# Kernel tuning notes

Measured on AMD Instinct MI355X. Metric: run time of the kernel, lower is better.

The kernel has to match this reference:

```python
import jax, jax.numpy as jnp
import numpy as np

H = 8          # n_heads
M = 16         # max_dist
U = 512        # n_units
DH = U // H    # d_head
EPS = 1e-3     # keras LayerNormalization default epsilon
NEG = -2.0**32 + 1.0


def _rel_table(pe, T):
    # pe: [2M+1, DH]; returns [T, T, DH] with rel[i, j] = pe[clip(j - i, -M, M) + M]
    i = jnp.arange(T)
    idx = jnp.clip(i[None, :] - i[:, None], -M, M) + M
    return pe[idx]


def _split_heads(x):
    # [B, T, U] -> [H*B, T, DH]  (head-major, matching tf.concat(tf.split(x, H, 2), 0))
    B, T, _ = x.shape
    return x.reshape(B, T, H, DH).transpose(2, 0, 1, 3).reshape(H * B, T, DH)


def _merge_heads(x, B):
    # [H*B, T, DH] -> [B, T, U]
    T = x.shape[1]
    return x.reshape(H, B, T, DH).transpose(1, 2, 0, 3).reshape(B, T, U)


def setup_inputs() -> dict:
    key = jax.random.key(0)
    ks = jax.random.split(key, 10)
    B, T = 8, 1024
    s = 1.0 / np.sqrt(U)
    inp = {
        'q': jax.random.normal(ks[0], (B, T, U), jnp.float32),
        'k': jax.random.normal(ks[1], (B, T, U), jnp.float32),
        'v': jax.random.normal(ks[2], (B, T, U), jnp.float32),
        'Wq': jax.random.normal(ks[3], (U, U), jnp.float32) * s,
        'bq': jnp.zeros((U,), jnp.float32),
        'Wk': jax.random.normal(ks[4], (U, U), jnp.float32) * s,
        'bk': jnp.zeros((U,), jnp.float32),
        'Wv': jax.random.normal(ks[5], (U, U), jnp.float32) * s,
        'bv': jnp.zeros((U,), jnp.float32),
        'Wo': jax.random.normal(ks[6], (U, U), jnp.float32) * s,
        'bo': jnp.zeros((U,), jnp.float32),
        'gamma': jnp.ones((U,), jnp.float32),
        'beta': jnp.zeros((U,), jnp.float32),
        'pe_k': jax.random.normal(ks[7], (2 * M + 1, DH), jnp.float32) * 0.05,
        'pe_v': jax.random.normal(ks[8], (2 * M + 1, DH), jnp.float32) * 0.05,
    }
    return inp


def reference(q, k, v, Wq, bq, Wk, bk, Wv, bv, Wo, bo, gamma, beta, pe_k, pe_v):
    B, T, _ = q.shape
    relu = jax.nn.relu
    q_emb = relu(q @ Wq + bq)
    k_emb = relu(k @ Wk + bk)
    v_emb = relu(v @ Wv + bv)
    qh = _split_heads(q_emb)   # [HB, T, DH]
    kh = _split_heads(k_emb)
    vh = _split_heads(v_emb)

    attn = jnp.einsum('btd,bsd->bts', qh, kh)
    rel_k = _rel_table(pe_k, T)                       # [T, T, DH]
    attn = attn + jnp.einsum('btd,tsd->bts', qh, rel_k)
    attn = attn / jnp.asarray(DH, attn.dtype) ** 0.5

    causal = jnp.tril(jnp.ones((T, T), jnp.bool_))
    attn = jnp.where(causal[None], attn, jnp.asarray(NEG, attn.dtype))
    w = jax.nn.softmax(attn, axis=-1)

    out = jnp.einsum('bts,bsd->btd', w, vh)
    rel_v = _rel_table(pe_v, T)
    out = out + jnp.einsum('bts,tsd->btd', w, rel_v)

    out = _merge_heads(out, B)                        # [B, T, U]
    out = relu(out @ Wo + bo)
    out = out + q

    mu = jnp.mean(out, axis=-1, keepdims=True)
    var = jnp.mean(jnp.square(out - mu), axis=-1, keepdims=True)
    return (out - mu) * jax.lax.rsqrt(var + EPS) * gamma + beta
```

## Files before the change

kernel.cpp:

```cpp
#include <hip/hip_runtime.h>
#include <hip/hip_bf16.h>

#define T_SEQ 1024
#define U_DIM 512
#define LN_EPS 1e-3f
#define LOG2E 1.44269504f

typedef float  f32x4  __attribute__((ext_vector_type(4)));
typedef short  bf16x8 __attribute__((ext_vector_type(8)));

__device__ __forceinline__ unsigned short f2bf(float f) {
    union { float f; unsigned u; } x; x.f = f;
    unsigned r = x.u + 0x7fffu + ((x.u >> 16) & 1u);
    return (unsigned short)(r >> 16);
}
__device__ __forceinline__ float b2f(short s) {
    union { unsigned u; float f; } x; x.u = ((unsigned)(unsigned short)s) << 16;
    return x.f;
}
__device__ __forceinline__ int packbf(float a, float b) {
    return (int)((unsigned)f2bf(a) | ((unsigned)f2bf(b) << 16));
}
__device__ __forceinline__ void async_copy16(void* lds, const void* g) {
    __builtin_amdgcn_global_load_lds((const __attribute__((address_space(1))) void*)g,
                                     (__attribute__((address_space(3))) void*)lds, 16, 0, 0);
}

#define WAITV(N) asm volatile("s_waitcnt vmcnt(" #N ")" ::: "memory")

__global__ __launch_bounds__(256) void prep_all(
        const float* __restrict__ Wq, const float* __restrict__ Wk,
        const float* __restrict__ Wv, const float* __restrict__ Wo,
        short* __restrict__ wt,
        const float* __restrict__ q, const float* __restrict__ k, const float* __restrict__ v,
        short* __restrict__ qb, short* __restrict__ kb, short* __restrict__ vb) {
    __shared__ float Ws[64][65];
    const int bid = blockIdx.x, t = threadIdx.x;
    if (bid >= 256) {
        const size_t off = ((size_t)(bid - 256) * 256 + t) * 8;
#pragma unroll
        for (int z = 0; z < 3; ++z) {
            const float* src = (z == 0) ? q : (z == 1) ? k : v;
            short* dst = (z == 0) ? qb : (z == 1) ? kb : vb;
            float4 a = *(const float4*)(src + off);
            float4 b = *(const float4*)(src + off + 4);
            int4 o;
            o.x = packbf(a.x, a.y);
            o.y = packbf(a.z, a.w);
            o.z = packbf(b.x, b.y);
            o.w = packbf(b.z, b.w);
            *(int4*)(dst + off) = o;
        }
        return;
    }
    const int z = bid >> 6, tile = bid & 63;
    const float* W = (z == 0) ? Wq : (z == 1) ? Wk : (z == 2) ? Wv : Wo;
    short* Wt = wt + (size_t)z * 262144;
    const int k0 = (tile >> 3) * 64, n0 = (tile & 7) * 64;
    {
        const int kr = t >> 2, cs = (t & 3) * 16;
        const float4* src = (const float4*)(W + (size_t)(k0 + kr) * 512 + n0 + cs);
#pragma unroll
        for (int i = 0; i < 4; ++i) {
            float4 vv = src[i];
            Ws[kr][cs + 4 * i + 0] = vv.x;
            Ws[kr][cs + 4 * i + 1] = vv.y;
            Ws[kr][cs + 4 * i + 2] = vv.z;
            Ws[kr][cs + 4 * i + 3] = vv.w;
        }
    }
    __syncthreads();
    {
        const int nr = t >> 2, ks = (t & 3) * 16;
        int4 w0, w1;
        w0.x = packbf(Ws[ks + 0][nr], Ws[ks + 1][nr]);
        w0.y = packbf(Ws[ks + 2][nr], Ws[ks + 3][nr]);
        w0.z = packbf(Ws[ks + 4][nr], Ws[ks + 5][nr]);
        w0.w = packbf(Ws[ks + 6][nr], Ws[ks + 7][nr]);
        w1.x = packbf(Ws[ks + 8][nr], Ws[ks + 9][nr]);
        w1.y = packbf(Ws[ks + 10][nr], Ws[ks + 11][nr]);
        w1.z = packbf(Ws[ks + 12][nr], Ws[ks + 13][nr]);
        w1.w = packbf(Ws[ks + 14][nr], Ws[ks + 15][nr]);
        short* dst = Wt + (size_t)(n0 + nr) * 512 + k0 + ks;
        *(int4*)dst = w0;
        *(int4*)(dst + 8) = w1;
    }
}

template <int OUT, int BM, int BN>
__global__ __launch_bounds__(256) void gemm_mfma(
        const void* __restrict__ A0, const void* __restrict__ A1, const void* __restrict__ A2,
        const short* __restrict__ Wt0, const short* __restrict__ Wt1, const short* __restrict__ Wt2,
        const float* __restrict__ b0p, const float* __restrict__ b1p, const float* __restrict__ b2p,
        const float* __restrict__ resid,
        void* __restrict__ O0, void* __restrict__ O1, void* __restrict__ O2) {
    constexpr int ASZ = BM * 32;
    constexpr int BSZ = BN * 32;
    constexpr int TSZ = ASZ + BSZ;
    constexpr int NA  = BM / 16;
    constexpr int NB  = BN / 16;
    constexpr int MW  = BM / 64;
    constexpr int NW  = 4 / MW;
    constexpr int AJ  = BN / (16 * NW);
    constexpr int LPW = (NA + NB) / 4;
    static_assert((NA + NB) % 4 == 0, "cells divisible by waves");
    __shared__ short Ls[4 * TSZ];

    const int z = blockIdx.z;
    const void* Av = (z == 0) ? A0 : (z == 1) ? A1 : A2;
    const short* Wz = (z == 0) ? Wt0 : (z == 1) ? Wt1 : Wt2;
    const float* bz = (z == 0) ? b0p : (z == 1) ? b1p : b2p;
    void* Ov = (z == 0) ? O0 : (z == 1) ? O1 : O2;

    const int tid = threadIdx.x;
    const int m0 = blockIdx.x * BM, n0 = blockIdx.y * BN;
    const int w = tid >> 6, lane = tid & 63;
    const int n15 = lane & 15, g = lane >> 4;
    const int mh = w / NW, nh = w % NW;

    f32x4 acc[4][AJ];
#pragma unroll
    for (int i = 0; i < 4; ++i)
#pragma unroll
        for (int j = 0; j < AJ; ++j) acc[i][j] = (f32x4){0.f, 0.f, 0.f, 0.f};

    const short* gsrc[LPW];
    int loff[LPW];
#pragma unroll
    for (int cl = 0; cl < LPW; ++cl) {
        const int cid = w * LPW + cl;
        if (cid < NA) {
            gsrc[cl] = (const short*)Av + (size_t)(m0 + cid * 16 + n15) * 512 + g * 8;
            loff[cl] = cid * 512;
        } else {
            const int c2 = cid - NA;
            gsrc[cl] = Wz + (size_t)(n0 + c2 * 16 + n15) * 512 + g * 8;
            loff[cl] = ASZ + c2 * 512;
        }
    }

#define STAGE(CK, BUF)                                                                   \
    do {                                                                                 \
        _Pragma("unroll")                                                                \
        for (int cl = 0; cl < LPW; ++cl)                                                 \
            async_copy16(Ls + (BUF) * TSZ + loff[cl], gsrc[cl] + (CK) * 32);             \
    } while (0)

    STAGE(0, 0);
    STAGE(1, 1);
    STAGE(2, 2);

    for (int ck = 0; ck < 16; ++ck) {
        if (ck < 14) {
            if constexpr (LPW == 3) WAITV(6); else WAITV(4);
        } else if (ck == 14) {
            if constexpr (LPW == 3) WAITV(3); else WAITV(2);
        } else {
            WAITV(0);
        }
        __builtin_amdgcn_s_barrier();
        __builtin_amdgcn_sched_barrier(0);
        if (ck + 3 <= 15) STAGE(ck + 3, (ck + 3) & 3);
        const int cb = ck & 3;
        bf16x8 af[4], bfv[AJ];
#pragma unroll
        for (int i = 0; i < 4; ++i)
            af[i] = *(const bf16x8*)(Ls + cb * TSZ + (mh * 4 + i) * 512 + lane * 8);
#pragma unroll
        for (int j = 0; j < AJ; ++j)
            bfv[j] = *(const bf16x8*)(Ls + cb * TSZ + ASZ + (nh * AJ + j) * 512 + lane * 8);
#pragma unroll
        for (int i = 0; i < 4; ++i)
#pragma unroll
            for (int j = 0; j < AJ; ++j)
                acc[i][j] = __builtin_amdgcn_mfma_f32_16x16x32_bf16(af[i], bfv[j], acc[i][j], 0, 0, 0);
    }
#undef STAGE

    const int mbase = m0 + mh * 64 + g * 4;
    const int nbase = n0 + nh * (AJ * 16) + n15;
    const bool even = (n15 & 1) == 0;
    float bj[AJ];
#pragma unroll
    for (int j = 0; j < AJ; ++j) bj[j] = bz[nbase + j * 16];

#pragma unroll
    for (int i = 0; i < 4; ++i) {
        const int mrow = mbase + i * 16;
#pragma unroll
        for (int j = 0; j < AJ; ++j) {
            const int ncol = nbase + j * 16;
            f32x4 a = acc[i][j];
            float v0 = fmaxf(a[0] + bj[j], 0.f);
            float v1 = fmaxf(a[1] + bj[j], 0.f);
            float v2 = fmaxf(a[2] + bj[j], 0.f);
            float v3 = fmaxf(a[3] + bj[j], 0.f);
            if (OUT == 0) {
                unsigned t01 = (unsigned)packbf(v0, v1);
                unsigned t23 = (unsigned)packbf(v2, v3);
                unsigned x01 = (unsigned)__shfl_xor((int)t01, 1, 64);
                unsigned x23 = (unsigned)__shfl_xor((int)t23, 1, 64);
                short* Oz = (short*)Ov;
                if (even) {
                    unsigned d0 = (t01 & 0xffffu) | (x01 << 16);
                    unsigned d1 = (t01 >> 16) | (x01 & 0xffff0000u);
                    *(unsigned*)(Oz + (size_t)(mrow + 0) * 512 + ncol) = d0;
                    *(unsigned*)(Oz + (size_t)(mrow + 1) * 512 + ncol) = d1;
                } else {
                    unsigned d2 = (x23 & 0xffffu) | (t23 << 16);
                    unsigned d3 = (x23 >> 16) | (t23 & 0xffff0000u);
                    *(unsigned*)(Oz + (size_t)(mrow + 2) * 512 + ncol - 1) = d2;
                    *(unsigned*)(Oz + (size_t)(mrow + 3) * 512 + ncol - 1) = d3;
                }
            } else {
                float x0 = __shfl_xor(v0, 1, 64);
                float x1 = __shfl_xor(v1, 1, 64);
                float x2 = __shfl_xor(v2, 1, 64);
                float x3 = __shfl_xor(v3, 1, 64);
                float* Oz = (float*)Ov;
                if (even) {
                    float2 r0 = *(const float2*)(resid + (size_t)(mrow + 0) * 512 + ncol);
                    float2 r1 = *(const float2*)(resid + (size_t)(mrow + 1) * 512 + ncol);
                    *(float2*)(Oz + (size_t)(mrow + 0) * 512 + ncol) = make_float2(v0 + r0.x, x0 + r0.y);
                    *(float2*)(Oz + (size_t)(mrow + 1) * 512 + ncol) = make_float2(v1 + r1.x, x1 + r1.y);
                } else {
                    float2 r2 = *(const float2*)(resid + (size_t)(mrow + 2) * 512 + ncol - 1);
                    float2 r3 = *(const float2*)(resid + (size_t)(mrow + 3) * 512 + ncol - 1);
                    *(float2*)(Oz + (size_t)(mrow + 2) * 512 + ncol - 1) = make_float2(x2 + r2.x, v2 + r2.y);
                    *(float2*)(Oz + (size_t)(mrow + 3) * 512 + ncol - 1) = make_float2(x3 + r3.x, v3 + r3.y);
                }
            }
        }
    }
}

__global__ __launch_bounds__(256) void attn_mfma(
        const short* __restrict__ qe, const short* __restrict__ ke,
        const short* __restrict__ ve, const float* __restrict__ pe_k,
        float* __restrict__ ml, short* __restrict__ ao) {
    __shared__ short Kc[2 * 4096];
    __shared__ short Vc[2 * 4096];
    __shared__ float qpeS[4 * 16 * 17];

    const int tid = threadIdx.x;
    const int bid = blockIdx.x;
    const int q4 = bid >> 8, r4 = bid & 3;
    const int rank = (q4 < 2) ? (r4 + 4 * q4) : (15 - (r4 + 4 * (q4 - 2)));
    const int hb = (bid >> 2) & 63;
    const int tt = 15 - rank;
    const int h = hb >> 3, b = hb & 7;
    const int w = tid >> 6, lane = tid & 63;
    const int g = lane >> 4, n15 = lane & 15;
    const int sp = tid & 31, dbase = (tid >> 5) * 8;
    float* qpeW = qpeS + w * (16 * 17);

    const size_t rowbase = (size_t)b * T_SEQ;

    int qn = 0;
    bf16x8 Bq[2];
    float qpe0 = 0.f;
    float m_r = -1.0e38f, l_r = 0.f, m2 = -1.4427e38f;
    f32x4 oacc[4];

#define SETUP(TILE)                                                                      \
    do {                                                                                 \
        qn = (TILE) * 64 + w * 16;                                                       \
        _Pragma("unroll")                                                                \
        for (int kh = 0; kh < 2; ++kh) {                                                 \
            bf16x8 t = *(const bf16x8*)(qe + (rowbase + qn + n15) * U_DIM + h * 64 + kh * 32 + g * 8); \
            _Pragma("unroll")                                                            \
            for (int i2 = 0; i2 < 8; ++i2) {                                             \
                unsigned short u = (unsigned short)t[i2];                                \
                t[i2] = (short)(((u & 0x7f80u) > 0x0180u) ? (unsigned short)(u - 0x0180u) \
                                                          : (unsigned short)(u & 0x8000u)); \
            }                                                                            \
            Bq[kh] = t;                                                                  \
        }                                                                                \
        f32x4 qa[2];                                                                     \
        qa[0] = (f32x4){0.f, 0.f, 0.f, 0.f};                                             \
        qa[1] = (f32x4){0.f, 0.f, 0.f, 0.f};                                             \
        _Pragma("unroll")                                                                \
        for (int mt = 0; mt < 2; ++mt)                                                   \
        _Pragma("unroll")                                                                \
        for (int kh = 0; kh < 2; ++kh) {                                                 \
            const float* src = pe_k + (mt * 16 + n15) * 64 + kh * 32 + g * 8;            \
            float4 f0 = *(const float4*)src;                                             \
            float4 f1 = *(const float4*)(src + 4);                                       \
            bf16x8 fr;                                                                   \
            fr[0] = (short)f2bf(f0.x); fr[1] = (short)f2bf(f0.y);                        \
            fr[2] = (short)f2bf(f0.z); fr[3] = (short)f2bf(f0.w);                        \
            fr[4] = (short)f2bf(f1.x); fr[5] = (short)f2bf(f1.y);                        \
            fr[6] = (short)f2bf(f1.z); fr[7] = (short)f2bf(f1.w);                        \
            qa[mt] = __builtin_amdgcn_mfma_f32_16x16x32_bf16(fr, Bq[kh], qa[mt], 0, 0, 0); \
        }                                                                                \
        _Pragma("unroll")                                                                \
        for (int mt = 0; mt < 2; ++mt)                                                   \
        _Pragma("unroll")                                                                \
        for (int r = 0; r < 4; ++r) {                                                    \
            const int ri = mt * 16 + 4 * g + r;                                          \
            if (ri <= 16) qpeW[n15 * 17 + ri] = qa[mt][r];                               \
        }                                                                                \
        qpe0 = qpeW[n15 * 17];                                                           \
        m_r = -1.0e38f; l_r = 0.f; m2 = -1.4427e38f;                                     \
        _Pragma("unroll")                                                                \
        for (int dt = 0; dt < 4; ++dt) oacc[dt] = (f32x4){0.f, 0.f, 0.f, 0.f};           \
    } while (0)

#define STAGE_K(S, BUF)                                                                  \
    do {                                                                                 \
        _Pragma("unroll")                                                                \
        for (int j = 0; j < 2; ++j) {                                                    \
            const int cc = w * 2 + j, kh = cc >> 2, mt = cc & 3;                         \
            const short* gp = ke + (rowbase + (S) + mt * 16 + n15) * U_DIM + h * 64 + kh * 32 + g * 8; \
            async_copy16(Kc + (BUF) * 4096 + cc * 512, gp);                              \
        }                                                                                \
    } while (0)

#define LOAD_V(S)                                                                        \
    do {                                                                                 \
        const short* r0 = ve + (rowbase + (S) + 2 * sp) * U_DIM + h * 64 + dbase;        \
        vx = *(const bf16x8*)r0;                                                         \
        vy = *(const bf16x8*)(r0 + U_DIM);                                               \
    } while (0)

#define STORE_V(BUF)                                                                     \
    do {                                                                                 \
        const int vkh = sp >> 4, vg = (sp & 15) >> 2, vj = (sp & 3) * 2;                 \
        _Pragma("unroll")                                                                \
        for (int i = 0; i < 8; ++i) {                                                    \
            const int d = dbase + i;                                                     \
            int pv = (int)((unsigned short)vx[i]) | (((int)(unsigned short)vy[i]) << 16);\
            *(int*)(Vc + (BUF) * 4096 + (vkh * 4 + (d >> 4)) * 512 + ((d & 15) + 16 * vg) * 8 + vj) = pv; \
        }                                                                                \
    } while (0)

    SETUP(tt);
    bf16x8 vx, vy;
    STAGE_K(0, 0);
    LOAD_V(0);
    STORE_V(0);

    for (int gs = 0; gs <= tt; ++gs) {
        const int cb = gs & 1, nb = cb ^ 1;
        const int s0 = gs * 64;
        __syncthreads();
        if (gs < tt) {
            STAGE_K((gs + 1) * 64, nb);
            LOAD_V((gs + 1) * 64);
        }

        {
            int cls[4];
#pragma unroll
            for (int mt = 0; mt < 4; ++mt) {
                const int slo = s0 + mt * 16;
                cls[mt] = (slo > qn + 15) ? 0 : ((slo + 31 < qn) ? 1 : 2);
            }
            f32x4 c[4];
#pragma unroll
            for (int mt = 0; mt < 4; ++mt) c[mt] = (f32x4){0.f, 0.f, 0.f, 0.f};
            __builtin_amdgcn_s_setprio(1);
#pragma unroll
            for (int mt = 0; mt < 4; ++mt) {
                if (!cls[mt]) continue;
#pragma unroll
                for (int kh = 0; kh < 2; ++kh) {
                    bf16x8 ak = *(const bf16x8*)(Kc + cb * 4096 + (kh * 4 + mt) * 512 + lane * 8);
                    c[mt] = __builtin_amdgcn_mfma_f32_16x16x32_bf16(ak, Bq[kh], c[mt], 0, 0, 0);
                }
            }
            __builtin_amdgcn_s_setprio(0);

            const int qg = qn + n15;
            float sc[4][4];
            float pmax = -3.0e38f;
#pragma unroll
            for (int mt = 0; mt < 4; ++mt) {
                if (cls[mt] == 0) {
#pragma unroll
                    for (int r = 0; r < 4; ++r) sc[mt][r] = -3.0e38f;
                } else if (cls[mt] == 1) {
#pragma unroll
                    for (int r = 0; r < 4; ++r) {
                        sc[mt][r] = c[mt][r] + qpe0;
                        pmax = fmaxf(pmax, sc[mt][r]);
                    }
                } else {
#pragma unroll
                    for (int r = 0; r < 4; ++r) {
                        const int sg = s0 + mt * 16 + 4 * g + r;
                        const int dlt = sg - qg;
                        if (dlt <= 0) {
                            const int ri = (dlt < -16) ? 0 : (dlt + 16);
                            sc[mt][r] = c[mt][r] + qpeW[n15 * 17 + ri];
                            pmax = fmaxf(pmax, sc[mt][r]);
                        } else {
                            sc[mt][r] = -3.0e38f;
                        }
                    }
                }
            }
            pmax = fmaxf(pmax, __shfl_xor(pmax, 16, 64));
            pmax = fmaxf(pmax, __shfl_xor(pmax, 32, 64));

            const bool resc = __any(pmax > m_r + 8.0f);
            float alpha = 1.0f;
            if (resc) {
                const float mnew = fmaxf(m_r, pmax);
                alpha = __expf(m_r - mnew);
                m_r = mnew;
                m2 = mnew * LOG2E;
            }
            float p[4][4];
            float psum = 0.f;
#pragma unroll
            for (int mt = 0; mt < 4; ++mt)
#pragma unroll
            for (int r = 0; r < 4; ++r) {
                const float pv = (cls[mt] == 0) ? 0.f
                                : exp2f(fmaf(sc[mt][r], LOG2E, -m2));
                p[mt][r] = pv;
                psum += pv;
            }
            psum += __shfl_xor(psum, 16, 64);
            psum += __shfl_xor(psum, 32, 64);
            l_r = l_r * alpha + psum;

            int pk01[4], pk23[4];
#pragma unroll
            for (int mt = 0; mt < 4; ++mt) {
                asm("v_cvt_pk_bf16_f32 %0, %1, %2" : "=v"(pk01[mt]) : "v"(p[mt][0]), "v"(p[mt][1]));
                asm("v_cvt_pk_bf16_f32 %0, %1, %2" : "=v"(pk23[mt]) : "v"(p[mt][2]), "v"(p[mt][3]));
            }
            const int srcA = ((g & 1) * 2) * 16 + n15;
            const int srcB = srcA + 16;
            const bool selHi = (g >> 1) != 0;
            if (resc) {
                float aO[4];
#pragma unroll
                for (int r = 0; r < 4; ++r) aO[r] = __shfl(alpha, 4 * g + r, 64);
#pragma unroll
                for (int dt = 0; dt < 4; ++dt)
#pragma unroll
                for (int r = 0; r < 4; ++r) oacc[dt][r] *= aO[r];
            }
#pragma unroll
            for (int kh = 0; kh < 2; ++kh) {
                if (cls[2 * kh] == 0 && cls[2 * kh + 1] == 0) continue;
                const int a0l = __shfl(pk01[2 * kh], srcA, 64);
                const int a0h = __shfl(pk01[2 * kh + 1], srcA, 64);
                const int a1l = __shfl(pk23[2 * kh], srcA, 64);
                const int a1h = __shfl(pk23[2 * kh + 1], srcA, 64);
                const int a2l = __shfl(pk01[2 * kh], srcB, 64);
                const int a2h = __shfl(pk01[2 * kh + 1], srcB, 64);
                const int a3l = __shfl(pk23[2 * kh], srcB, 64);
                const int a3h = __shfl(pk23[2 * kh + 1], srcB, 64);
                union { int i[4]; bf16x8 v; } au;
                au.i[0] = selHi ? a0h : a0l;
                au.i[1] = selHi ? a1h : a1l;
                au.i[2] = selHi ? a2h : a2l;
                au.i[3] = selHi ? a3h : a3l;
                __builtin_amdgcn_s_setprio(1);
#pragma unroll
                for (int dt = 0; dt < 4; ++dt) {
                    bf16x8 bv = *(const bf16x8*)(Vc + cb * 4096 + (kh * 4 + dt) * 512 + lane * 8);
                    oacc[dt] = __builtin_amdgcn_mfma_f32_16x16x32_bf16(au.v, bv, oacc[dt], 0, 0, 0);
                }
                __builtin_amdgcn_s_setprio(0);
            }
        }

        if (gs < tt) STORE_V(nb);
    }

    if (g == 0)
        *(float2*)(ml + ((size_t)hb * T_SEQ + qn + n15) * 2) = make_float2(m_r, l_r);
#pragma unroll
    for (int r = 0; r < 4; ++r) {
        const float lq = __shfl(l_r, 4 * g + r, 64);
        const float linv = 1.0f / lq;
        short* dst = ao + (rowbase + qn + 4 * g + r) * U_DIM + h * 64 + n15;
#pragma unroll
        for (int dt = 0; dt < 4; ++dt)
            dst[dt * 16] = (short)f2bf(oacc[dt][r] * linv);
    }
#undef SETUP
#undef STAGE_K
#undef LOAD_V
#undef STORE_V
}

__global__ __launch_bounds__(256) void band_relv(
        const short* __restrict__ qe, const short* __restrict__ ke,
        const float* __restrict__ pe_k, const float* __restrict__ pe_v,
        const float* __restrict__ ml, short* __restrict__ ao) {
    __shared__ float pek[17 * 64];
    __shared__ float pev[17 * 64];
    const int tb = blockIdx.x, hb = blockIdx.y;
    const int h = hb >> 3, b = hb & 7;
    const int tid = threadIdx.x;
    for (int i = tid; i < 17 * 64; i += 256) {
        pek[i] = b2f((short)f2bf(pe_k[i]));
        pev[i] = pe_v[i];
    }
    __syncthreads();

    const int t = tb * 64 + (tid >> 2);
    const int p = (tid & 3) * 16;
    const short* qp = qe + (size_t)(b * T_SEQ + t) * U_DIM + h * 64 + p;
    bf16x8 qa = *(const bf16x8*)qp, qb2 = *(const bf16x8*)(qp + 8);
    float qv[16];
#pragma unroll
    for (int i = 0; i < 8; ++i) { qv[i] = b2f(qa[i]); qv[8 + i] = b2f(qb2[i]); }

    float dots[17];
#pragma unroll
    for (int ri = 0; ri < 17; ++ri) {
        const int s = t - 16 + ri;
        float acc = 0.f;
        if (s >= 0) {
            const short* kp = ke + (size_t)(b * T_SEQ + s) * U_DIM + h * 64 + p;
            bf16x8 ka = *(const bf16x8*)kp, kb2 = *(const bf16x8*)(kp + 8);
#pragma unroll
            for (int d = 0; d < 8; ++d) {
                acc += qv[d] * b2f(ka[d]);
                acc += qv[8 + d] * b2f(kb2[d]);
            }
#pragma unroll
            for (int d = 0; d < 16; ++d) acc += qv[d] * pek[ri * 64 + p + d];
        }
        dots[ri] = acc;
    }
#pragma unroll
    for (int ri = 0; ri < 17; ++ri) {
        dots[ri] += __shfl_xor(dots[ri], 1, 64);
        dots[ri] += __shfl_xor(dots[ri], 2, 64);
    }

    const float2 mlv = *(const float2*)(ml + ((size_t)hb * T_SEQ + t) * 2);
    const float m = mlv.x, linv = 1.0f / mlv.y;
    float wv[17];
    float wsum = 0.f;
#pragma unroll
    for (int ri = 0; ri < 17; ++ri) {
        const int s = t - 16 + ri;
        const float wr = (s >= 0) ? __expf(dots[ri] * 0.125f - m) * linv : 0.f;
        wv[ri] = wr;
        wsum += wr;
    }
    wv[0] += 1.0f - wsum;

    float relv[16];
#pragma unroll
    for (int d = 0; d < 16; ++d) relv[d] = 0.f;
#pragma unroll
    for (int ri = 0; ri < 17; ++ri)
#pragma unroll
        for (int d = 0; d < 16; ++d) relv[d] += wv[ri] * pev[ri * 64 + p + d];

    short* op = ao + (size_t)(b * T_SEQ + t) * U_DIM + h * 64 + p;
    bf16x8 a0 = *(const bf16x8*)op, a1 = *(const bf16x8*)(op + 8);
    int4 o0, o1;
    o0.x = packbf(b2f(a0[0]) + relv[0],  b2f(a0[1]) + relv[1]);
    o0.y = packbf(b2f(a0[2]) + relv[2],  b2f(a0[3]) + relv[3]);
    o0.z = packbf(b2f(a0[4]) + relv[4],  b2f(a0[5]) + relv[5]);
    o0.w = packbf(b2f(a0[6]) + relv[6],  b2f(a0[7]) + relv[7]);
    o1.x = packbf(b2f(a1[0]) + relv[8],  b2f(a1[1]) + relv[9]);
    o1.y = packbf(b2f(a1[2]) + relv[10], b2f(a1[3]) + relv[11]);
    o1.z = packbf(b2f(a1[4]) + relv[12], b2f(a1[5]) + relv[13]);
    o1.w = packbf(b2f(a1[6]) + relv[14], b2f(a1[7]) + relv[15]);
    *(int4*)op = o0;
    *(int4*)(op + 8) = o1;
}

__global__ __launch_bounds__(256) void ln_kernel(float* __restrict__ io,
                                                 const float* __restrict__ gamma,
                                                 const float* __restrict__ beta) {
    const int row = blockIdx.x * 4 + (threadIdx.x >> 6);
    const int lane = threadIdx.x & 63;
    float* rp = io + (size_t)row * 512 + lane * 8;
    float4 a = *(const float4*)rp;
    float4 c = *(const float4*)(rp + 4);
    float v[8] = {a.x, a.y, a.z, a.w, c.x, c.y, c.z, c.w};

    float s = v[0] + v[1] + v[2] + v[3] + v[4] + v[5] + v[6] + v[7];
#pragma unroll
    for (int off = 1; off < 64; off <<= 1) s += __shfl_xor(s, off, 64);
    const float mu = s * (1.0f / 512.0f);

    float sq = 0.f;
#pragma unroll
    for (int i = 0; i < 8; ++i) { v[i] -= mu; sq += v[i] * v[i]; }
#pragma unroll
    for (int off = 1; off < 64; off <<= 1) sq += __shfl_xor(sq, off, 64);
    const float rs = rsqrtf(sq * (1.0f / 512.0f) + LN_EPS);

    const float4 g0 = *(const float4*)(gamma + lane * 8);
    const float4 g1 = *(const float4*)(gamma + lane * 8 + 4);
    const float4 b0 = *(const float4*)(beta + lane * 8);
    const float4 b1 = *(const float4*)(beta + lane * 8 + 4);
    float4 o0, o1;
    o0.x = v[0] * rs * g0.x + b0.x;
    o0.y = v[1] * rs * g0.y + b0.y;
    o0.z = v[2] * rs * g0.z + b0.z;
    o0.w = v[3] * rs * g0.w + b0.w;
    o1.x = v[4] * rs * g1.x + b1.x;
    o1.y = v[5] * rs * g1.y + b1.y;
    o1.z = v[6] * rs * g1.z + b1.z;
    o1.w = v[7] * rs * g1.w + b1.w;
    *(float4*)rp = o0;
    *(float4*)(rp + 4) = o1;
}

extern "C" void kernel_launch(void* const* d_in, const int* in_sizes, int n_in,
                              void* d_out, int out_size, void* d_ws, size_t ws_size,
                              hipStream_t stream) {
    const float* q     = (const float*)d_in[0];
    const float* k     = (const float*)d_in[1];
    const float* v     = (const float*)d_in[2];
    const float* Wq    = (const float*)d_in[3];
    const float* bq    = (const float*)d_in[4];
    const float* Wk    = (const float*)d_in[5];
    const float* bk    = (const float*)d_in[6];
    const float* Wv    = (const float*)d_in[7];
    const float* bv    = (const float*)d_in[8];
    const float* Wo    = (const float*)d_in[9];
    const float* bo    = (const float*)d_in[10];
    const float* gamma = (const float*)d_in[11];
    const float* beta  = (const float*)d_in[12];
    const float* pe_k  = (const float*)d_in[13];
    const float* pe_v  = (const float*)d_in[14];
    float* out = (float*)d_out;

    char* base = (char*)d_ws;
    short* qe = (short*)(base);
    short* ke = (short*)(base + (((size_t)8) << 20));
    short* ve = (short*)(base + (((size_t)16) << 20));
    short* ao = (short*)(base + (((size_t)24) << 20));
    short* wt = (short*)(base + (((size_t)32) << 20));
    float* ml = (float*)(base + (((size_t)34) << 20));
    short* qb = (short*)(base + (((size_t)36) << 20));
    short* kb = (short*)(base + (((size_t)44) << 20));
    short* vb = (short*)(base + (((size_t)52) << 20));
    short* wtq = wt, *wtk = wt + 262144, *wtv = wt + 2 * 262144, *wto = wt + 3 * 262144;

    prep_all<<<dim3(2304), 256, 0, stream>>>(Wq, Wk, Wv, Wo, wt, q, k, v, qb, kb, vb);
    gemm_mfma<0, 128, 64><<<dim3(64, 8, 3), 256, 0, stream>>>(
        qb, kb, vb, wtq, wtk, wtv, bq, bk, bv, nullptr, qe, ke, ve);
    attn_mfma<<<dim3(1024), 256, 0, stream>>>(qe, ke, ve, pe_k, ml, ao);
    band_relv<<<dim3(16, 64), 256, 0, stream>>>(qe, ke, pe_k, pe_v, ml, ao);
    gemm_mfma<1, 64, 64><<<dim3(128, 8, 1), 256, 0, stream>>>(
        ao, ao, ao, wto, wto, wto, bo, bo, bo, q, out, out, out);
    ln_kernel<<<dim3(2048), 256, 0, stream>>>(out, gamma, beta);
}
```

Measured before the change: 252.6 us.

## Split attention KV range across two blocks per query tile and combine

Each query tile's causal key range is split into two halves handled by separate blocks (flash-decoding style split-K), doubling the grid to 2048 blocks for better load balance across CUs. A new combine kernel merges the partial outputs using the per-row max and sum statistics, writing the merged ml for band_relv. The output GEMM tile shape also changes to 64x128 with half the grid. This adds an extra kernel launch plus global traffic for the partial results, and reuses the qb/kb buffers as scratch.

```diff
diff --git a/kernel.cpp b/kernel.cpp
--- a/kernel.cpp
+++ b/kernel.cpp
@@ -237,17 +237,23 @@
 __global__ __launch_bounds__(256) void attn_mfma(
         const short* __restrict__ qe, const short* __restrict__ ke,
         const short* __restrict__ ve, const float* __restrict__ pe_k,
-        float* __restrict__ ml, short* __restrict__ ao) {
+        float* __restrict__ ml1, float* __restrict__ ml2,
+        short* __restrict__ ao, short* __restrict__ ao2) {
     __shared__ short Kc[2 * 4096];
     __shared__ short Vc[2 * 4096];
     __shared__ float qpeS[4 * 16 * 17];
 
     const int tid = threadIdx.x;
     const int bid = blockIdx.x;
-    const int q4 = bid >> 8, r4 = bid & 3;
-    const int rank = (q4 < 2) ? (r4 + 4 * q4) : (15 - (r4 + 4 * (q4 - 2)));
-    const int hb = (bid >> 2) & 63;
-    const int tt = 15 - rank;
+    const int cu = bid & 255, chunk = bid >> 8;
+    const int hb = cu >> 2, r4 = cu & 3;
+    int tt, half;
+    if (chunk < 4) { tt = 4 * r4 + chunk;              half = 0; }
+    else           { tt = 15 - 4 * r4 - (chunk - 4);   half = 1; }
+    const int n0h = (tt + 2) >> 1;
+    const int g0 = half ? n0h : 0;
+    const int g1 = half ? (tt + 1) : n0h;
+
     const int h = hb >> 3, b = hb & 7;
     const int w = tid >> 6, lane = tid & 63;
     const int g = lane >> 4, n15 = lane & 15;
@@ -255,56 +261,62 @@
     float* qpeW = qpeS + w * (16 * 17);
 
     const size_t rowbase = (size_t)b * T_SEQ;
-
-    int qn = 0;
+    short* aoP = half ? ao2 : ao;
+    float* mlP = half ? ml2 : ml1;
+
+    int qn = tt * 64 + w * 16;
+
+    if (g0 >= g1) {
+        if (g == 0)
+            *(float2*)(mlP + ((size_t)hb * T_SEQ + qn + n15) * 2) = make_float2(-3.0e38f, 0.f);
+        return;
+    }
+
     bf16x8 Bq[2];
     float qpe0 = 0.f;
     float m_r = -1.0e38f, l_r = 0.f, m2 = -1.4427e38f;
     f32x4 oacc[4];
 
-#define SETUP(TILE)                                                                      \
-    do {                                                                                 \
-        qn = (TILE) * 64 + w * 16;                                                       \
-        _Pragma("unroll")                                                                \
-        for (int kh = 0; kh < 2; ++kh) {                                                 \
-            bf16x8 t = *(const bf16x8*)(qe + (rowbase + qn + n15) * U_DIM + h * 64 + kh * 32 + g * 8); \
-            _Pragma("unroll")                                                            \
-            for (int i2 = 0; i2 < 8; ++i2) {                                             \
-                unsigned short u = (unsigned short)t[i2];                                \
-                t[i2] = (short)(((u & 0x7f80u) > 0x0180u) ? (unsigned short)(u - 0x0180u) \
-                                                          : (unsigned short)(u & 0x8000u)); \
-            }                                                                            \
-            Bq[kh] = t;                                                                  \
-        }                                                                                \
-        f32x4 qa[2];                                                                     \
-        qa[0] = (f32x4){0.f, 0.f, 0.f, 0.f};                                             \
-        qa[1] = (f32x4){0.f, 0.f, 0.f, 0.f};                                             \
-        _Pragma("unroll")                                                                \
-        for (int mt = 0; mt < 2; ++mt)                                                   \
-        _Pragma("unroll")                                                                \
-        for (int kh = 0; kh < 2; ++kh) {                                                 \
-            const float* src = pe_k + (mt * 16 + n15) * 64 + kh * 32 + g * 8;            \
-            float4 f0 = *(const float4*)src;                                             \
-            float4 f1 = *(const float4*)(src + 4);                                       \
-            bf16x8 fr;                                                                   \
-            fr[0] = (short)f2bf(f0.x); fr[1] = (short)f2bf(f0.y);                        \
-            fr[2] = (short)f2bf(f0.z); fr[3] = (short)f2bf(f0.w);                        \
-            fr[4] = (short)f2bf(f1.x); fr[5] = (short)f2bf(f1.y);                        \
-            fr[6] = (short)f2bf(f1.z); fr[7] = (short)f2bf(f1.w);                        \
-            qa[mt] = __builtin_amdgcn_mfma_f32_16x16x32_bf16(fr, Bq[kh], qa[mt], 0, 0, 0); \
-        }                                                                                \
-        _Pragma("unroll")                                                                \
-        for (int mt = 0; mt < 2; ++mt)                                                   \
-        _Pragma("unroll")                                                                \
-        for (int r = 0; r < 4; ++r) {                                                    \
-            const int ri = mt * 16 + 4 * g + r;                                          \
-            if (ri <= 16) qpeW[n15 * 17 + ri] = qa[mt][r];                               \
-        }                                                                                \
-        qpe0 = qpeW[n15 * 17];                                                           \
-        m_r = -1.0e38f; l_r = 0.f; m2 = -1.4427e38f;                                     \
-        _Pragma("unroll")                                                                \
-        for (int dt = 0; dt < 4; ++dt) oacc[dt] = (f32x4){0.f, 0.f, 0.f, 0.f};           \
-    } while (0)
+    {
+#pragma unroll
+        for (int kh = 0; kh < 2; ++kh) {
+            bf16x8 t = *(const bf16x8*)(qe + (rowbase + qn + n15) * U_DIM + h * 64 + kh * 32 + g * 8);
+#pragma unroll
+            for (int i2 = 0; i2 < 8; ++i2) {
+                unsigned short u = (unsigned short)t[i2];
+                t[i2] = (short)(((u & 0x7f80u) > 0x0180u) ? (unsigned short)(u - 0x0180u)
+                                                          : (unsigned short)(u & 0x8000u));
+            }
+            Bq[kh] = t;
+        }
+        f32x4 qa[2];
+        qa[0] = (f32x4){0.f, 0.f, 0.f, 0.f};
+        qa[1] = (f32x4){0.f, 0.f, 0.f, 0.f};
+#pragma unroll
+        for (int mt = 0; mt < 2; ++mt)
+#pragma unroll
+        for (int kh = 0; kh < 2; ++kh) {
+            const float* src = pe_k + (mt * 16 + n15) * 64 + kh * 32 + g * 8;
+            float4 f0 = *(const float4*)src;
+            float4 f1 = *(const float4*)(src + 4);
+            bf16x8 fr;
+            fr[0] = (short)f2bf(f0.x); fr[1] = (short)f2bf(f0.y);
+            fr[2] = (short)f2bf(f0.z); fr[3] = (short)f2bf(f0.w);
+            fr[4] = (short)f2bf(f1.x); fr[5] = (short)f2bf(f1.y);
+            fr[6] = (short)f2bf(f1.z); fr[7] = (short)f2bf(f1.w);
+            qa[mt] = __builtin_amdgcn_mfma_f32_16x16x32_bf16(fr, Bq[kh], qa[mt], 0, 0, 0);
+        }
+#pragma unroll
+        for (int mt = 0; mt < 2; ++mt)
+#pragma unroll
+        for (int r = 0; r < 4; ++r) {
+            const int ri = mt * 16 + 4 * g + r;
+            if (ri <= 16) qpeW[n15 * 17 + ri] = qa[mt][r];
+        }
+        qpe0 = qpeW[n15 * 17];
+#pragma unroll
+        for (int dt = 0; dt < 4; ++dt) oacc[dt] = (f32x4){0.f, 0.f, 0.f, 0.f};
+    }
 
 #define STAGE_K(S, BUF)                                                                  \
     do {                                                                                 \
@@ -334,17 +346,16 @@
         }                                                                                \
     } while (0)
 
-    SETUP(tt);
     bf16x8 vx, vy;
-    STAGE_K(0, 0);
-    LOAD_V(0);
-    STORE_V(0);
-
-    for (int gs = 0; gs <= tt; ++gs) {
+    STAGE_K(g0 * 64, g0 & 1);
+    LOAD_V(g0 * 64);
+    STORE_V(g0 & 1);
+
+    for (int gs = g0; gs < g1; ++gs) {
         const int cb = gs & 1, nb = cb ^ 1;
         const int s0 = gs * 64;
         __syncthreads();
-        if (gs < tt) {
+        if (gs + 1 < g1) {
             STAGE_K((gs + 1) * 64, nb);
             LOAD_V((gs + 1) * 64);
         }
@@ -470,24 +481,63 @@
             }
         }
 
-        if (gs < tt) STORE_V(nb);
+        if (gs + 1 < g1) STORE_V(nb);
     }
 
     if (g == 0)
-        *(float2*)(ml + ((size_t)hb * T_SEQ + qn + n15) * 2) = make_float2(m_r, l_r);
+        *(float2*)(mlP + ((size_t)hb * T_SEQ + qn + n15) * 2) = make_float2(m_r, l_r);
 #pragma unroll
     for (int r = 0; r < 4; ++r) {
         const float lq = __shfl(l_r, 4 * g + r, 64);
-        const float linv = 1.0f / lq;
-        short* dst = ao + (rowbase + qn + 4 * g + r) * U_DIM + h * 64 + n15;
+        const float linv = (lq > 0.f) ? 1.0f / lq : 0.f;
+        short* dst = aoP + (rowbase + qn + 4 * g + r) * U_DIM + h * 64 + n15;
 #pragma unroll
         for (int dt = 0; dt < 4; ++dt)
             dst[dt * 16] = (short)f2bf(oacc[dt][r] * linv);
     }
-#undef SETUP
 #undef STAGE_K
 #undef LOAD_V
 #undef STORE_V
+}
+
+__global__ __launch_bounds__(256) void attn_combine(
+        const float* __restrict__ ml1, const float* __restrict__ ml2,
+        const short* __restrict__ ao2, short* __restrict__ ao,
+        float* __restrict__ ml) {
+    const int R = blockIdx.x * 64 + (threadIdx.x >> 2);
+    const int hb = R >> 10, t = R & 1023;
+    const int h = hb >> 3, b = hb & 7;
+    const int d0 = (threadIdx.x & 3) * 16;
+    const float2 p1 = *(const float2*)(ml1 + (size_t)R * 2);
+    const float2 p2 = *(const float2*)(ml2 + (size_t)R * 2);
+    const float m = fmaxf(p1.x, p2.x);
+    const float w1 = p1.y * __expf(p1.x - m);
+    const float w2 = (p2.y > 0.f) ? p2.y * __expf(p2.x - m) : 0.f;
+    const float inv = 1.0f / (w1 + w2);
+    const float a1 = w1 * inv, a2 = w2 * inv;
+    const size_t off = (size_t)(b * T_SEQ + t) * U_DIM + h * 64 + d0;
+    short* op = ao + off;
+    const short* o2p = ao2 + off;
+    bf16x8 x0 = *(const bf16x8*)op, x1 = *(const bf16x8*)(op + 8);
+    bf16x8 y0 = *(const bf16x8*)o2p, y1 = *(const bf16x8*)(o2p + 8);
+    const bool has2 = (w2 > 0.f);
+    float o[16];
+#pragma unroll
+    for (int i = 0; i < 8; ++i) {
+        float t0 = a1 * b2f(x0[i]);
+        float t1 = a1 * b2f(x1[i]);
+        o[i]     = has2 ? (t0 + a2 * b2f(y0[i])) : t0;
+        o[8 + i] = has2 ? (t1 + a2 * b2f(y1[i])) : t1;
+    }
+    int4 o0, o1;
+    o0.x = packbf(o[0], o[1]);   o0.y = packbf(o[2], o[3]);
+    o0.z = packbf(o[4], o[5]);   o0.w = packbf(o[6], o[7]);
+    o1.x = packbf(o[8], o[9]);   o1.y = packbf(o[10], o[11]);
+    o1.z = packbf(o[12], o[13]); o1.w = packbf(o[14], o[15]);
+    *(int4*)op = o0;
+    *(int4*)(op + 8) = o1;
+    if ((threadIdx.x & 3) == 0)
+        *(float2*)(ml + (size_t)R * 2) = make_float2(m, w1 + w2);
 }
 
 __global__ __launch_bounds__(256) void band_relv(
@@ -639,17 +689,21 @@
     short* ao = (short*)(base + (((size_t)24) << 20));
     short* wt = (short*)(base + (((size_t)32) << 20));
     float* ml = (float*)(base + (((size_t)34) << 20));
+    float* ml1 = (float*)(base + (((size_t)35) << 20));
     short* qb = (short*)(base + (((size_t)36) << 20));
     short* kb = (short*)(base + (((size_t)44) << 20));
     short* vb = (short*)(base + (((size_t)52) << 20));
+    short* ao2 = qb;
+    float* ml2 = (float*)kb;
     short* wtq = wt, *wtk = wt + 262144, *wtv = wt + 2 * 262144, *wto = wt + 3 * 262144;
 
     prep_all<<<dim3(2304), 256, 0, stream>>>(Wq, Wk, Wv, Wo, wt, q, k, v, qb, kb, vb);
     gemm_mfma<0, 128, 64><<<dim3(64, 8, 3), 256, 0, stream>>>(
         qb, kb, vb, wtq, wtk, wtv, bq, bk, bv, nullptr, qe, ke, ve);
-    attn_mfma<<<dim3(1024), 256, 0, stream>>>(qe, ke, ve, pe_k, ml, ao);
+    attn_mfma<<<dim3(2048), 256, 0, stream>>>(qe, ke, ve, pe_k, ml1, ml2, ao, ao2);
+    attn_combine<<<dim3(1024), 256, 0, stream>>>(ml1, ml2, ao2, ao, ml);
     band_relv<<<dim3(16, 64), 256, 0, stream>>>(qe, ke, pe_k, pe_v, ml, ao);
-    gemm_mfma<1, 64, 64><<<dim3(128, 8, 1), 256, 0, stream>>>(
+    gemm_mfma<1, 64, 128><<<dim3(128, 4, 1), 256, 0, stream>>>(
         ao, ao, ao, wto, wto, wto, bo, bo, bo, q, out, out, out);
     ln_kernel<<<dim3(2048), 256, 0, stream>>>(out, gamma, beta);
 }
```

After: 262.0 us. 1.04x slower.

## Fuse fp32-to-bf16 input conversion into QKV projection GEMM

Applied to the files above, without the earlier changes.

Removes the separate pass that converted q/k/v to bf16 and instead loads fp32 activations directly in a new GEMM kernel. That kernel converts them to bf16 in registers while staging into LDS, double-buffered against async weight loads, with 128x128 tiles. The output projection becomes a dedicated non-template-branch kernel with a 64x128 tile, and the attention setup macro is inlined. This saves one full write and read of the bf16 activation copies, but the A path now uses register-staged loads instead of async copies.

```diff
diff --git a/kernel.cpp b/kernel.cpp
--- a/kernel.cpp
+++ b/kernel.cpp
@@ -28,31 +28,12 @@
 
 #define WAITV(N) asm volatile("s_waitcnt vmcnt(" #N ")" ::: "memory")
 
-__global__ __launch_bounds__(256) void prep_all(
+__global__ __launch_bounds__(256) void prep_wt(
         const float* __restrict__ Wq, const float* __restrict__ Wk,
         const float* __restrict__ Wv, const float* __restrict__ Wo,
-        short* __restrict__ wt,
-        const float* __restrict__ q, const float* __restrict__ k, const float* __restrict__ v,
-        short* __restrict__ qb, short* __restrict__ kb, short* __restrict__ vb) {
+        short* __restrict__ wt) {
     __shared__ float Ws[64][65];
     const int bid = blockIdx.x, t = threadIdx.x;
-    if (bid >= 256) {
-        const size_t off = ((size_t)(bid - 256) * 256 + t) * 8;
-#pragma unroll
-        for (int z = 0; z < 3; ++z) {
-            const float* src = (z == 0) ? q : (z == 1) ? k : v;
-            short* dst = (z == 0) ? qb : (z == 1) ? kb : vb;
-            float4 a = *(const float4*)(src + off);
-            float4 b = *(const float4*)(src + off + 4);
-            int4 o;
-            o.x = packbf(a.x, a.y);
-            o.y = packbf(a.z, a.w);
-            o.z = packbf(b.x, b.y);
-            o.w = packbf(b.z, b.w);
-            *(int4*)(dst + off) = o;
-        }
-        return;
-    }
     const int z = bid >> 6, tile = bid & 63;
     const float* W = (z == 0) ? Wq : (z == 1) ? Wk : (z == 2) ? Wv : Wo;
     short* Wt = wt + (size_t)z * 262144;
@@ -87,13 +68,142 @@
     }
 }
 
-template <int OUT, int BM, int BN>
-__global__ __launch_bounds__(256) void gemm_mfma(
-        const void* __restrict__ A0, const void* __restrict__ A1, const void* __restrict__ A2,
+__global__ __launch_bounds__(256) void gemm_cvt(
+        const float* __restrict__ A0, const float* __restrict__ A1, const float* __restrict__ A2,
         const short* __restrict__ Wt0, const short* __restrict__ Wt1, const short* __restrict__ Wt2,
         const float* __restrict__ b0p, const float* __restrict__ b1p, const float* __restrict__ b2p,
-        const float* __restrict__ resid,
-        void* __restrict__ O0, void* __restrict__ O1, void* __restrict__ O2) {
+        short* __restrict__ O0, short* __restrict__ O1, short* __restrict__ O2) {
+    __shared__ short As[2 * 8192];
+    __shared__ short Bs[2 * 8192];
+
+    const int z = blockIdx.z;
+    const float* Av = (z == 0) ? A0 : (z == 1) ? A1 : A2;
+    const short* Wz = (z == 0) ? Wt0 : (z == 1) ? Wt1 : Wt2;
+    const float* bz = (z == 0) ? b0p : (z == 1) ? b1p : b2p;
+    short* Ov = (z == 0) ? O0 : (z == 1) ? O1 : O2;
+
+    const int tid = threadIdx.x;
+    const int m0 = blockIdx.x * 128, n0 = blockIdx.y * 128;
+    const int w = tid >> 6, lane = tid & 63;
+    const int n15 = lane & 15, g = lane >> 4;
+    const int mh = w >> 1, nh = w & 1;
+    const int lr = tid >> 4, c4 = tid & 15;
+
+    f32x4 acc[4][4];
+#pragma unroll
+    for (int i = 0; i < 4; ++i)
+#pragma unroll
+        for (int j = 0; j < 4; ++j) acc[i][j] = (f32x4){0.f, 0.f, 0.f, 0.f};
+
+    float4 areg[8];
+
+#define LOAD_A(CK)                                                                       \
+    do {                                                                                 \
+        const float* abase = Av + (size_t)(m0 + lr) * 512 + (CK) * 64 + c4 * 4;          \
+        _Pragma("unroll")                                                                \
+        for (int i = 0; i < 8; ++i) areg[i] = *(const float4*)(abase + (size_t)8192 * i); \
+    } while (0)
+
+#define STORE_A(BUF)                                                                     \
+    do {                                                                                 \
+        short* sb = As + (BUF) * 8192 + (c4 >> 3) * 8 * 512 + lr * 8 +                   \
+                    ((c4 & 7) >> 1) * 128 + (c4 & 1) * 4;                                \
+        _Pragma("unroll")                                                                \
+        for (int i = 0; i < 8; ++i) {                                                    \
+            int2 wv;                                                                     \
+            wv.x = packbf(areg[i].x, areg[i].y);                                         \
+            wv.y = packbf(areg[i].z, areg[i].w);                                         \
+            *(int2*)(sb + i * 512) = wv;                                                 \
+        }                                                                                \
+    } while (0)
+
+#define STAGE_B(CK, BUF)                                                                 \
+    do {                                                                                 \
+        if (w < 2) {                                                                     \
+            _Pragma("unroll")                                                            \
+            for (int i = 0; i < 8; ++i) {                                                \
+                const int kc = i >> 2, nt = w * 4 + (i & 3);                             \
+                const short* gp = Wz + (size_t)(n0 + nt * 16 + n15) * 512 + (CK) * 64 + kc * 32 + g * 8; \
+                async_copy16(Bs + (BUF) * 8192 + (kc * 8 + nt) * 512, gp);               \
+            }                                                                            \
+        }                                                                                \
+    } while (0)
+
+    LOAD_A(0);
+    STORE_A(0);
+    STAGE_B(0, 0);
+    LOAD_A(1);
+
+    for (int ck = 0; ck < 8; ++ck) {
+        const int cb = ck & 1, nb = cb ^ 1;
+        __syncthreads();
+        if (ck < 7) STAGE_B(ck + 1, nb);
+#pragma unroll
+        for (int kc = 0; kc < 2; ++kc) {
+            bf16x8 af[4], bfv[4];
+#pragma unroll
+            for (int i = 0; i < 4; ++i)
+                af[i] = *(const bf16x8*)(As + cb * 8192 + (kc * 8 + mh * 4 + i) * 512 + lane * 8);
+#pragma unroll
+            for (int j = 0; j < 4; ++j)
+                bfv[j] = *(const bf16x8*)(Bs + cb * 8192 + (kc * 8 + nh * 4 + j) * 512 + lane * 8);
+#pragma unroll
+            for (int i = 0; i < 4; ++i)
+#pragma unroll
+                for (int j = 0; j < 4; ++j)
+                    acc[i][j] = __builtin_amdgcn_mfma_f32_16x16x32_bf16(af[i], bfv[j], acc[i][j], 0, 0, 0);
+        }
+        if (ck < 7) {
+            STORE_A(nb);
+            if (ck < 6) LOAD_A(ck + 2);
+        }
+    }
+#undef LOAD_A
+#undef STORE_A
+#undef STAGE_B
+
+    const int mbase = m0 + mh * 64 + g * 4;
+    const int nbase = n0 + nh * 64 + n15;
+    const bool even = (n15 & 1) == 0;
+    float bj[4];
+#pragma unroll
+    for (int j = 0; j < 4; ++j) bj[j] = bz[nbase + j * 16];
+
+#pragma unroll
+    for (int i = 0; i < 4; ++i) {
+        const int mrow = mbase + i * 16;
+#pragma unroll
+        for (int j = 0; j < 4; ++j) {
+            const int ncol = nbase + j * 16;
+            f32x4 a = acc[i][j];
+            float v0 = fmaxf(a[0] + bj[j], 0.f);
+            float v1 = fmaxf(a[1] + bj[j], 0.f);
+            float v2 = fmaxf(a[2] + bj[j], 0.f);
+            float v3 = fmaxf(a[3] + bj[j], 0.f);
+            unsigned t01 = (unsigned)packbf(v0, v1);
+            unsigned t23 = (unsigned)packbf(v2, v3);
+            unsigned x01 = (unsigned)__shfl_xor((int)t01, 1, 64);
+            unsigned x23 = (unsigned)__shfl_xor((int)t23, 1, 64);
+            if (even) {
+                unsigned d0 = (t01 & 0xffffu) | (x01 << 16);
+                unsigned d1 = (t01 >> 16) | (x01 & 0xffff0000u);
+                *(unsigned*)(Ov + (size_t)(mrow + 0) * 512 + ncol) = d0;
+                *(unsigned*)(Ov + (size_t)(mrow + 1) * 512 + ncol) = d1;
+            } else {
+                unsigned d2 = (x23 & 0xffffu) | (t23 << 16);
+                unsigned d3 = (x23 >> 16) | (t23 & 0xffff0000u);
+                *(unsigned*)(Ov + (size_t)(mrow + 2) * 512 + ncol - 1) = d2;
+                *(unsigned*)(Ov + (size_t)(mrow + 3) * 512 + ncol - 1) = d3;
+            }
+        }
+    }
+}
+
+template <int BM, int BN>
+__global__ __launch_bounds__(256) void gemm_pipe(
+        const short* __restrict__ Ab, const short* __restrict__ Wz,
+        const float* __restrict__ bz, const float* __restrict__ resid,
+        float* __restrict__ Oz) {
     constexpr int ASZ = BM * 32;
     constexpr int BSZ = BN * 32;
     constexpr int TSZ = ASZ + BSZ;
@@ -106,12 +216,6 @@
     static_assert((NA + NB) % 4 == 0, "cells divisible by waves");
     __shared__ short Ls[4 * TSZ];
 
-    const int z = blockIdx.z;
-    const void* Av = (z == 0) ? A0 : (z == 1) ? A1 : A2;
-    const short* Wz = (z == 0) ? Wt0 : (z == 1) ? Wt1 : Wt2;
-    const float* bz = (z == 0) ? b0p : (z == 1) ? b1p : b2p;
-    void* Ov = (z == 0) ? O0 : (z == 1) ? O1 : O2;
-
     const int tid = threadIdx.x;
     const int m0 = blockIdx.x * BM, n0 = blockIdx.y * BN;
     const int w = tid >> 6, lane = tid & 63;
@@ -130,7 +234,7 @@
     for (int cl = 0; cl < LPW; ++cl) {
         const int cid = w * LPW + cl;
         if (cid < NA) {
-            gsrc[cl] = (const short*)Av + (size_t)(m0 + cid * 16 + n15) * 512 + g * 8;
+            gsrc[cl] = Ab + (size_t)(m0 + cid * 16 + n15) * 512 + g * 8;
             loff[cl] = cid * 512;
         } else {
             const int c2 = cid - NA;
@@ -195,40 +299,20 @@
             float v1 = fmaxf(a[1] + bj[j], 0.f);
             float v2 = fmaxf(a[2] + bj[j], 0.f);
             float v3 = fmaxf(a[3] + bj[j], 0.f);
-            if (OUT == 0) {
-                unsigned t01 = (unsigned)packbf(v0, v1);
-                unsigned t23 = (unsigned)packbf(v2, v3);
-                unsigned x01 = (unsigned)__shfl_xor((int)t01, 1, 64);
-                unsigned x23 = (unsigned)__shfl_xor((int)t23, 1, 64);
-                short* Oz = (short*)Ov;
-                if (even) {
-                    unsigned d0 = (t01 & 0xffffu) | (x01 << 16);
-                    unsigned d1 = (t01 >> 16) | (x01 & 0xffff0000u);
-                    *(unsigned*)(Oz + (size_t)(mrow + 0) * 512 + ncol) = d0;
-                    *(unsigned*)(Oz + (size_t)(mrow + 1) * 512 + ncol) = d1;
-                } else {
-                    unsigned d2 = (x23 & 0xffffu) | (t23 << 16);
-                    unsigned d3 = (x23 >> 16) | (t23 & 0xffff0000u);
-                    *(unsigned*)(Oz + (size_t)(mrow + 2) * 512 + ncol - 1) = d2;
-                    *(unsigned*)(Oz + (size_t)(mrow + 3) * 512 + ncol - 1) = d3;
-                }
+            float x0 = __shfl_xor(v0, 1, 64);
+            float x1 = __shfl_xor(v1, 1, 64);
+            float x2 = __shfl_xor(v2, 1, 64);
+            float x3 = __shfl_xor(v3, 1, 64);
+            if (even) {
+                float2 r0 = *(const float2*)(resid + (size_t)(mrow + 0) * 512 + ncol);
+                float2 r1 = *(const float2*)(resid + (size_t)(mrow + 1) * 512 + ncol);
+                *(float2*)(Oz + (size_t)(mrow + 0) * 512 + ncol) = make_float2(v0 + r0.x, x0 + r0.y);
+                *(float2*)(Oz + (size_t)(mrow + 1) * 512 + ncol) = make_float2(v1 + r1.x, x1 + r1.y);
             } else {
-                float x0 = __shfl_xor(v0, 1, 64);
-                float x1 = __shfl_xor(v1, 1, 64);
-                float x2 = __shfl_xor(v2, 1, 64);
-                float x3 = __shfl_xor(v3, 1, 64);
-                float* Oz = (float*)Ov;
-                if (even) {
-                    float2 r0 = *(const float2*)(resid + (size_t)(mrow + 0) * 512 + ncol);
-                    float2 r1 = *(const float2*)(resid + (size_t)(mrow + 1) * 512 + ncol);
-                    *(float2*)(Oz + (size_t)(mrow + 0) * 512 + ncol) = make_float2(v0 + r0.x, x0 + r0.y);
-                    *(float2*)(Oz + (size_t)(mrow + 1) * 512 + ncol) = make_float2(v1 + r1.x, x1 + r1.y);
-                } else {
-                    float2 r2 = *(const float2*)(resid + (size_t)(mrow + 2) * 512 + ncol - 1);
-                    float2 r3 = *(const float2*)(resid + (size_t)(mrow + 3) * 512 + ncol - 1);
-                    *(float2*)(Oz + (size_t)(mrow + 2) * 512 + ncol - 1) = make_float2(x2 + r2.x, v2 + r2.y);
-                    *(float2*)(Oz + (size_t)(mrow + 3) * 512 + ncol - 1) = make_float2(x3 + r3.x, v3 + r3.y);
-                }
+                float2 r2 = *(const float2*)(resid + (size_t)(mrow + 2) * 512 + ncol - 1);
+                float2 r3 = *(const float2*)(resid + (size_t)(mrow + 3) * 512 + ncol - 1);
+                *(float2*)(Oz + (size_t)(mrow + 2) * 512 + ncol - 1) = make_float2(x2 + r2.x, v2 + r2.y);
+                *(float2*)(Oz + (size_t)(mrow + 3) * 512 + ncol - 1) = make_float2(x3 + r3.x, v3 + r3.y);
             }
         }
     }
@@ -256,55 +340,52 @@
 
     const size_t rowbase = (size_t)b * T_SEQ;
 
-    int qn = 0;
+    const int qn = tt * 64 + w * 16;
     bf16x8 Bq[2];
     float qpe0 = 0.f;
     float m_r = -1.0e38f, l_r = 0.f, m2 = -1.4427e38f;
     f32x4 oacc[4];
 
-#define SETUP(TILE)                                                                      \
-    do {                                                                                 \
-        qn = (TILE) * 64 + w * 16;                                                       \
-        _Pragma("unroll")                                                                \
-        for (int kh = 0; kh < 2; ++kh) {                                                 \
-            bf16x8 t = *(const bf16x8*)(qe + (rowbase + qn + n15) * U_DIM + h * 64 + kh * 32 + g * 8); \
-            _Pragma("unroll")                                                            \
-            for (int i2 = 0; i2 < 8; ++i2) {                                             \
-                unsigned short u = (unsigned short)t[i2];                                \
-                t[i2] = (short)(((u & 0x7f80u) > 0x0180u) ? (unsigned short)(u - 0x0180u) \
-                                                          : (unsigned short)(u & 0x8000u)); \
-            }                                                                            \
-            Bq[kh] = t;                                                                  \
-        }                                                                                \
-        f32x4 qa[2];                                                                     \
-        qa[0] = (f32x4){0.f, 0.f, 0.f, 0.f};                                             \
-        qa[1] = (f32x4){0.f, 0.f, 0.f, 0.f};                                             \
-        _Pragma("unroll")                                                                \
-        for (int mt = 0; mt < 2; ++mt)                                                   \
-        _Pragma("unroll")                                                                \
-        for (int kh = 0; kh < 2; ++kh) {                                                 \
-            const float* src = pe_k + (mt * 16 + n15) * 64 + kh * 32 + g * 8;            \
-            float4 f0 = *(const float4*)src;                                             \
-            float4 f1 = *(const float4*)(src + 4);                                       \
-            bf16x8 fr;                                                                   \
-            fr[0] = (short)f2bf(f0.x); fr[1] = (short)f2bf(f0.y);                        \
-            fr[2] = (short)f2bf(f0.z); fr[3] = (short)f2bf(f0.w);                        \
-            fr[4] = (short)f2bf(f1.x); fr[5] = (short)f2bf(f1.y);                        \
-            fr[6] = (short)f2bf(f1.z); fr[7] = (short)f2bf(f1.w);                        \
-            qa[mt] = __builtin_amdgcn_mfma_f32_16x16x32_bf16(fr, Bq[kh], qa[mt], 0, 0, 0); \
-        }                                                                                \
-        _Pragma("unroll")                                                                \
-        for (int mt = 0; mt < 2; ++mt)                                                   \
-        _Pragma("unroll")                                                                \
-        for (int r = 0; r < 4; ++r) {                                                    \
-            const int ri = mt * 16 + 4 * g + r;                                          \
-            if (ri <= 16) qpeW[n15 * 17 + ri] = qa[mt][r];                               \
-        }                                                                                \
-        qpe0 = qpeW[n15 * 17];                                                           \
-        m_r = -1.0e38f; l_r = 0.f; m2 = -1.4427e38f;                                     \
-        _Pragma("unroll")                                                                \
-        for (int dt = 0; dt < 4; ++dt) oacc[dt] = (f32x4){0.f, 0.f, 0.f, 0.f};           \
-    } while (0)
+    {
+#pragma unroll
+        for (int kh = 0; kh < 2; ++kh) {
+            bf16x8 t = *(const bf16x8*)(qe + (rowbase + qn + n15) * U_DIM + h * 64 + kh * 32 + g * 8);
+#pragma unroll
+            for (int i2 = 0; i2 < 8; ++i2) {
+                unsigned short u = (unsigned short)t[i2];
+                t[i2] = (short)(((u & 0x7f80u) > 0x0180u) ? (unsigned short)(u - 0x0180u)
+                                                          : (unsigned short)(u & 0x8000u));
+            }
+            Bq[kh] = t;
+        }
+        f32x4 qa[2];
+        qa[0] = (f32x4){0.f, 0.f, 0.f, 0.f};
+        qa[1] = (f32x4){0.f, 0.f, 0.f, 0.f};
+#pragma unroll
+        for (int mt = 0; mt < 2; ++mt)
+#pragma unroll
+        for (int kh = 0; kh < 2; ++kh) {
+            const float* src = pe_k + (mt * 16 + n15) * 64 + kh * 32 + g * 8;
+            float4 f0 = *(const float4*)src;
+            float4 f1 = *(const float4*)(src + 4);
+            bf16x8 fr;
+            fr[0] = (short)f2bf(f0.x); fr[1] = (short)f2bf(f0.y);
+            fr[2] = (short)f2bf(f0.z); fr[3] = (short)f2bf(f0.w);
+            fr[4] = (short)f2bf(f1.x); fr[5] = (short)f2bf(f1.y);
+            fr[6] = (short)f2bf(f1.z); fr[7] = (short)f2bf(f1.w);
+            qa[mt] = __builtin_amdgcn_mfma_f32_16x16x32_bf16(fr, Bq[kh], qa[mt], 0, 0, 0);
+        }
+#pragma unroll
+        for (int mt = 0; mt < 2; ++mt)
+#pragma unroll
+        for (int r = 0; r < 4; ++r) {
+            const int ri = mt * 16 + 4 * g + r;
+            if (ri <= 16) qpeW[n15 * 17 + ri] = qa[mt][r];
+        }
+        qpe0 = qpeW[n15 * 17];
+#pragma unroll
+        for (int dt = 0; dt < 4; ++dt) oacc[dt] = (f32x4){0.f, 0.f, 0.f, 0.f};
+    }
 
 #define STAGE_K(S, BUF)                                                                  \
     do {                                                                                 \
@@ -334,7 +415,6 @@
         }                                                                                \
     } while (0)
 
-    SETUP(tt);
     bf16x8 vx, vy;
     STAGE_K(0, 0);
     LOAD_V(0);
@@ -484,7 +564,6 @@
         for (int dt = 0; dt < 4; ++dt)
             dst[dt * 16] = (short)f2bf(oacc[dt][r] * linv);
     }
-#undef SETUP
 #undef STAGE_K
 #undef LOAD_V
 #undef STORE_V
@@ -639,17 +718,13 @@
     short* ao = (short*)(base + (((size_t)24) << 20));
     short* wt = (short*)(base + (((size_t)32) << 20));
     float* ml = (float*)(base + (((size_t)34) << 20));
-    short* qb = (short*)(base + (((size_t)36) << 20));
-    short* kb = (short*)(base + (((size_t)44) << 20));
-    short* vb = (short*)(base + (((size_t)52) << 20));
     short* wtq = wt, *wtk = wt + 262144, *wtv = wt + 2 * 262144, *wto = wt + 3 * 262144;
 
-    prep_all<<<dim3(2304), 256, 0, stream>>>(Wq, Wk, Wv, Wo, wt, q, k, v, qb, kb, vb);
-    gemm_mfma<0, 128, 64><<<dim3(64, 8, 3), 256, 0, stream>>>(
-        qb, kb, vb, wtq, wtk, wtv, bq, bk, bv, nullptr, qe, ke, ve);
+    prep_wt<<<dim3(256), 256, 0, stream>>>(Wq, Wk, Wv, Wo, wt);
+    gemm_cvt<<<dim3(64, 4, 3), 256, 0, stream>>>(
+        q, k, v, wtq, wtk, wtv, bq, bk, bv, qe, ke, ve);
     attn_mfma<<<dim3(1024), 256, 0, stream>>>(qe, ke, ve, pe_k, ml, ao);
     band_relv<<<dim3(16, 64), 256, 0, stream>>>(qe, ke, pe_k, pe_v, ml, ao);
-    gemm_mfma<1, 64, 64><<<dim3(128, 8, 1), 256, 0, stream>>>(
-        ao, ao, ao, wto, wto, wto, bo, bo, bo, q, out, out, out);
+    gemm_pipe<64, 128><<<dim3(128, 4), 256, 0, stream>>>(ao, wto, bo, q, out);
     ln_kernel<<<dim3(2048), 256, 0, stream>>>(out, gamma, beta);
 }
```

Result: faster. 239.7 us (-5.1%).
